# Kernel optimization log

Hardware: AMD Instinct MI355X
Metric: run time of the kernel (lower is better)

Reference implementation:

```python
import jax, jax.numpy as jnp
import numpy as np

B, S, D, H, E, F = 4, 2048, 1024, 16, 8, 4096
CAP_FACTOR = 1.25
DH = D // H


def setup_inputs() -> dict:
    key = jax.random.key(0)
    ks = jax.random.split(key, 8)
    s = 0.02
    return {
        "src": jax.random.normal(ks[0], (B, S, D), jnp.float32),
        "src_pad_mask": jnp.zeros((B, S), jnp.bool_),  # True = padding
        "ln1_g": jnp.ones((D,), jnp.float32),
        "ln1_b": jnp.zeros((D,), jnp.float32),
        "in_proj_w": jax.random.normal(ks[1], (3 * D, D), jnp.float32) * s,
        "in_proj_b": jnp.zeros((3 * D,), jnp.float32),
        "out_proj_w": jax.random.normal(ks[2], (D, D), jnp.float32) * s,
        "out_proj_b": jnp.zeros((D,), jnp.float32),
        "ln2_g": jnp.ones((D,), jnp.float32),
        "ln2_b": jnp.zeros((D,), jnp.float32),
        "router_w": jax.random.normal(ks[3], (D, E), jnp.float32) * s,
        "router_b": jnp.zeros((E,), jnp.float32),
        "w1": jax.random.normal(ks[4], (E, D, F), jnp.float32) * s,
        "b1": jnp.zeros((E, F), jnp.float32),
        "w2": jax.random.normal(ks[5], (E, F, D), jnp.float32) * s,
        "b2": jnp.zeros((E, D), jnp.float32),
    }


def _layernorm(x, g, b, eps=1e-5):
    m = jnp.mean(x, axis=-1, keepdims=True)
    v = jnp.mean(jnp.square(x - m), axis=-1, keepdims=True)
    return (x - m) * jax.lax.rsqrt(v + eps) * g + b


def _mha(x, pad_mask, in_proj_w, in_proj_b, out_proj_w, out_proj_b):
    qkv = x @ in_proj_w.T + in_proj_b                      # [B,S,3D]
    q, k, v = jnp.split(qkv, 3, axis=-1)
    q = q.reshape(B, S, H, DH)
    k = k.reshape(B, S, H, DH)
    v = v.reshape(B, S, H, DH)
    scores = jnp.einsum('bqhd,bkhd->bhqk', q, k) / np.sqrt(DH).astype(np.float32)
    scores = jnp.where(pad_mask[:, None, None, :], jnp.float32(-1e9), scores)
    attn = jax.nn.softmax(scores, axis=-1)
    out = jnp.einsum('bhqk,bkhd->bqhd', attn, v).reshape(B, S, D)
    return out @ out_proj_w.T + out_proj_b


def _switch(x, token_mask, router_w, router_b, w1, b1, w2, b2):
    N = B * S
    cap = int(CAP_FACTOR * N / E)
    tokens = x.reshape(N, D)
    tm = token_mask.reshape(N).astype(jnp.float32)
    logits = tokens @ router_w + router_b                  # [N,E]
    probs = jax.nn.softmax(logits, axis=-1)
    eidx = jnp.argmax(probs, axis=-1)                      # [N] top-1 expert
    gate = jnp.take_along_axis(probs, eidx[:, None], axis=1)[:, 0]
    oh = jax.nn.one_hot(eidx, E, dtype=jnp.float32) * tm[:, None]
    # position of each token within its expert's queue (1-based; 0 if masked)
    pos = jnp.sum(jnp.cumsum(oh, axis=0) * oh, axis=-1)
    keep = (pos > 0) & (pos <= cap)
    slot = eidx * cap + (pos - 1).astype(jnp.int32)        # flat slot in [E*cap)
    slot_scatter = jnp.where(keep, slot, E * cap)          # out-of-range => dropped
    keepf = keep.astype(jnp.float32)
    dispatch = jnp.zeros((E * cap, D), jnp.float32).at[slot_scatter].set(
        tokens * keepf[:, None], mode='drop')
    d = dispatch.reshape(E, cap, D)
    h = jax.nn.relu(jnp.einsum('ecd,edf->ecf', d, w1) + b1[:, None, :])
    o = jnp.einsum('ecf,efd->ecd', h, w2) + b2[:, None, :]
    slot_gather = jnp.where(keep, slot, 0)
    out = o.reshape(E * cap, D)[slot_gather] * (gate * keepf)[:, None]
    # aux losses over valid tokens
    denom = jnp.maximum(jnp.sum(tm), 1.0)
    f = jnp.sum(oh, axis=0) / denom                        # dispatch fraction per expert
    P = jnp.sum(probs * tm[:, None], axis=0) / denom       # mean router prob per expert
    lb_loss = E * jnp.sum(f * P)
    z_loss = jnp.sum(jnp.square(jax.nn.logsumexp(logits, axis=-1)) * tm) / denom
    return out.reshape(B, S, D), lb_loss, z_loss


def reference(src, src_pad_mask, ln1_g, ln1_b, in_proj_w, in_proj_b,
              out_proj_w, out_proj_b, ln2_g, ln2_b, router_w, router_b,
              w1, b1, w2, b2):
    x = _layernorm(src, ln1_g, ln1_b)
    attn = _mha(x, src_pad_mask, in_proj_w, in_proj_b, out_proj_w, out_proj_b)
    src1 = src + attn                                      # dropout=0.0
    token_mask = ~src_pad_mask
    x2 = _layernorm(src1, ln2_g, ln2_b)
    ffn, lb_loss, z_loss = _switch(x2, token_mask, router_w, router_b, w1, b1, w2, b2)
    src2 = src1 + ffn
    return (src2, lb_loss, z_loss)
```

## Files before the change

kernel.cpp:

```cpp
#include <hip/hip_runtime.h>

constexpr int cB = 4, cS = 2048, cD = 1024, cH = 16, cE = 8, cF = 4096;
constexpr int cN = cB * cS;
constexpr int cDH = 64;
constexpr int cCAP = 1280;

typedef __attribute__((ext_vector_type(8))) short bf16x8;
typedef __attribute__((ext_vector_type(4))) float f32x4;
typedef __attribute__((ext_vector_type(4))) unsigned short u16x4;
typedef __attribute__((ext_vector_type(4))) unsigned int u32x4;

__device__ inline unsigned short bf16_rne(float x) {
  unsigned u = __float_as_uint(x);
  u += 0x7FFF + ((u >> 16) & 1);
  return (unsigned short)(u >> 16);
}
__device__ inline float bf16_f(unsigned short h) {
  return __uint_as_float(((unsigned)h) << 16);
}
__device__ inline unsigned cvt_pk_bf16(float a, float b) {
  unsigned r;
  asm("v_cvt_pk_bf16_f32 %0, %1, %2" : "=v"(r) : "v"(a), "v"(b));
  return r;
}

__global__ __launch_bounds__(256) void ln_kernel(const float* __restrict__ x,
                                                 const float* __restrict__ g,
                                                 const float* __restrict__ bb,
                                                 float* __restrict__ y) {
  __shared__ float red[8];
  const int row = blockIdx.x;
  const int t = threadIdx.x;
  const float4 v = ((const float4*)(x + (size_t)row * cD))[t];
  float s = v.x + v.y + v.z + v.w;
#pragma unroll
  for (int m = 32; m >= 1; m >>= 1) s += __shfl_xor(s, m, 64);
  if ((t & 63) == 0) red[t >> 6] = s;
  __syncthreads();
  const float mean = (red[0] + red[1] + red[2] + red[3]) * (1.0f / cD);
  const float dx = v.x - mean, dy = v.y - mean, dz = v.z - mean, dw = v.w - mean;
  float ss = dx * dx + dy * dy + dz * dz + dw * dw;
#pragma unroll
  for (int m = 32; m >= 1; m >>= 1) ss += __shfl_xor(ss, m, 64);
  if ((t & 63) == 0) red[4 + (t >> 6)] = ss;
  __syncthreads();
  const float var = (red[4] + red[5] + red[6] + red[7]) * (1.0f / cD);
  const float inv = rsqrtf(var + 1e-5f);
  const float4 gg = ((const float4*)g)[t];
  const float4 b4 = ((const float4*)bb)[t];
  float4 o;
  o.x = dx * inv * gg.x + b4.x;
  o.y = dy * inv * gg.y + b4.y;
  o.z = dz * inv * gg.z + b4.z;
  o.w = dw * inv * gg.w + b4.w;
  ((float4*)(y + (size_t)row * cD))[t] = o;
}

__global__ __launch_bounds__(256) void ln_split_kernel(
    const float* __restrict__ x, const float* __restrict__ g,
    const float* __restrict__ bb, unsigned short* __restrict__ yh,
    unsigned short* __restrict__ yl) {
  __shared__ float red[8];
  const int row = blockIdx.x;
  const int t = threadIdx.x;
  const float4 v = ((const float4*)(x + (size_t)row * cD))[t];
  float s = v.x + v.y + v.z + v.w;
#pragma unroll
  for (int m = 32; m >= 1; m >>= 1) s += __shfl_xor(s, m, 64);
  if ((t & 63) == 0) red[t >> 6] = s;
  __syncthreads();
  const float mean = (red[0] + red[1] + red[2] + red[3]) * (1.0f / cD);
  const float dx = v.x - mean, dy = v.y - mean, dz = v.z - mean, dw = v.w - mean;
  float ss = dx * dx + dy * dy + dz * dz + dw * dw;
#pragma unroll
  for (int m = 32; m >= 1; m >>= 1) ss += __shfl_xor(ss, m, 64);
  if ((t & 63) == 0) red[4 + (t >> 6)] = ss;
  __syncthreads();
  const float var = (red[4] + red[5] + red[6] + red[7]) * (1.0f / cD);
  const float inv = rsqrtf(var + 1e-5f);
  const float4 gg = ((const float4*)g)[t];
  const float4 b4 = ((const float4*)bb)[t];
  const float oa[4] = {dx * inv * gg.x + b4.x, dy * inv * gg.y + b4.y,
                       dz * inv * gg.z + b4.z, dw * inv * gg.w + b4.w};
  u16x4 hh, ll;
#pragma unroll
  for (int i = 0; i < 4; i++) {
    const unsigned short h16 = bf16_rne(oa[i]);
    hh[i] = h16;
    ll[i] = bf16_rne(oa[i] - bf16_f(h16));
  }
  *(u16x4*)(yh + (size_t)row * cD + t * 4) = hh;
  *(u16x4*)(yl + (size_t)row * cD + t * 4) = ll;
}

__global__ __launch_bounds__(256) void wsplit_kernel(const float* __restrict__ in,
                                                     unsigned short* __restrict__ hi,
                                                     unsigned short* __restrict__ lo,
                                                     int n4) {
  const int i = blockIdx.x * 256 + threadIdx.x;
  if (i >= n4) return;
  const float4 v = ((const float4*)in)[i];
  const float a[4] = {v.x, v.y, v.z, v.w};
  u16x4 hh, ll;
#pragma unroll
  for (int j = 0; j < 4; j++) {
    const unsigned short h16 = bf16_rne(a[j]);
    hh[j] = h16;
    ll[j] = bf16_rne(a[j] - bf16_f(h16));
  }
  *(u16x4*)(hi + (size_t)i * 4) = hh;
  *(u16x4*)(lo + (size_t)i * 4) = ll;
}

__global__ __launch_bounds__(256) void padmask_kernel(
    const unsigned char* __restrict__ pad, float* __restrict__ mkf) {
  const int i = blockIdx.x * 256 + threadIdx.x;
  mkf[i] = pad[i] ? -1e30f : 0.0f;
}

__global__ __launch_bounds__(256) void transpose_bf16_kernel(
    const float* __restrict__ in, unsigned short* __restrict__ outp, int Rr,
    int Cc) {
  __shared__ float T[64][65];
  const int z = blockIdx.z;
  in += (size_t)z * Rr * Cc;
  outp += (size_t)z * Rr * Cc;
  const int c0 = blockIdx.x * 64, r0 = blockIdx.y * 64;
  const int tid = threadIdx.x;
#pragma unroll
  for (int u = 0; u < 4; u++) {
    const int a = tid + u * 256;
    const int r = a >> 4, c4 = (a & 15) << 2;
    const float4 v = *(const float4*)(in + (size_t)(r0 + r) * Cc + c0 + c4);
    T[r][c4 + 0] = v.x;
    T[r][c4 + 1] = v.y;
    T[r][c4 + 2] = v.z;
    T[r][c4 + 3] = v.w;
  }
  __syncthreads();
#pragma unroll
  for (int u = 0; u < 4; u++) {
    const int a = tid + u * 256;
    const int c = a >> 4, r4 = (a & 15) << 2;
    u16x4 o;
#pragma unroll
    for (int i = 0; i < 4; i++) o[i] = bf16_rne(T[r4 + i][c]);
    *(u16x4*)(outp + (size_t)(c0 + c) * Rr + r0 + r4) = o;
  }
}

template <bool SPLIT, bool RELU, bool RESID, int OUT>
__global__ __launch_bounds__(256) void gemm_bf16(
    const unsigned short* __restrict__ Ah, const unsigned short* __restrict__ Al,
    size_t sA,
    const unsigned short* __restrict__ Bh, const unsigned short* __restrict__ Bl,
    size_t sB,
    const float* __restrict__ bias, size_t sBias,
    const float* __restrict__ R,
    void* __restrict__ Cv, size_t sC,
    int K, int lda, int ldb, int ldc,
    unsigned short* __restrict__ Qh, unsigned short* __restrict__ Ql,
    unsigned short* __restrict__ Kh, unsigned short* __restrict__ Kl,
    unsigned short* __restrict__ Vth, unsigned short* __restrict__ Vtl) {
  __shared__ unsigned short AsH[128 * 40];
  __shared__ unsigned short BsH[128 * 40];
  __shared__ unsigned short AsL[SPLIT ? 128 * 40 : 8];
  __shared__ unsigned short BsL[SPLIT ? 128 * 40 : 8];
  const int z = blockIdx.z;
  Ah += (size_t)z * sA;
  Bh += (size_t)z * sB;
  if constexpr (SPLIT) {
    Al += (size_t)z * sA;
    Bl += (size_t)z * sB;
  }
  bias += (size_t)z * sBias;
  const int n0 = blockIdx.x * 128, m0 = blockIdx.y * 128;
  const int tid = threadIdx.x;
  const int wid = tid >> 6, lane = tid & 63;
  const int ln = lane & 15, quad = lane >> 4;
  const int wm = (wid >> 1) * 64, wn = (wid & 1) * 64;

  f32x4 acc[4][4];
#pragma unroll
  for (int i = 0; i < 4; i++)
#pragma unroll
    for (int j = 0; j < 4; j++) acc[i][j] = (f32x4){0.f, 0.f, 0.f, 0.f};

  for (int k0 = 0; k0 < K; k0 += 32) {
    __syncthreads();
#pragma unroll
    for (int u = 0; u < 2; u++) {
      const int c = tid + u * 256;
      const int row = c >> 2, ko = (c & 3) << 3;
      const int ld = row * 40 + ko;
      *(uint4*)&AsH[ld] = *(const uint4*)(Ah + (size_t)(m0 + row) * lda + k0 + ko);
      *(uint4*)&BsH[ld] = *(const uint4*)(Bh + (size_t)(n0 + row) * ldb + k0 + ko);
      if constexpr (SPLIT) {
        *(uint4*)&AsL[ld] = *(const uint4*)(Al + (size_t)(m0 + row) * lda + k0 + ko);
        *(uint4*)&BsL[ld] = *(const uint4*)(Bl + (size_t)(n0 + row) * ldb + k0 + ko);
      }
    }
    __syncthreads();
    bf16x8 bh[4], bl[4];
#pragma unroll
    for (int nt = 0; nt < 4; nt++) {
      bh[nt] = *(const bf16x8*)&BsH[(wn + nt * 16 + ln) * 40 + quad * 8];
      if constexpr (SPLIT)
        bl[nt] = *(const bf16x8*)&BsL[(wn + nt * 16 + ln) * 40 + quad * 8];
    }
#pragma unroll
    for (int mt = 0; mt < 4; mt++) {
      const bf16x8 ah = *(const bf16x8*)&AsH[(wm + mt * 16 + ln) * 40 + quad * 8];
      bf16x8 al;
      if constexpr (SPLIT)
        al = *(const bf16x8*)&AsL[(wm + mt * 16 + ln) * 40 + quad * 8];
#pragma unroll
      for (int nt = 0; nt < 4; nt++) {
        acc[mt][nt] =
            __builtin_amdgcn_mfma_f32_16x16x32_bf16(ah, bh[nt], acc[mt][nt], 0, 0, 0);
        if constexpr (SPLIT) {
          acc[mt][nt] =
              __builtin_amdgcn_mfma_f32_16x16x32_bf16(al, bh[nt], acc[mt][nt], 0, 0, 0);
          acc[mt][nt] =
              __builtin_amdgcn_mfma_f32_16x16x32_bf16(ah, bl[nt], acc[mt][nt], 0, 0, 0);
        }
      }
    }
  }
  if constexpr (OUT == 2) {
#pragma unroll
    for (int mt = 0; mt < 4; mt++) {
      const int row0 = m0 + wm + mt * 16 + quad * 4;
      const int b_ = row0 >> 11, s0_ = row0 & 2047;
      const size_t bbase = (size_t)b_ * cH * cS * cDH;
#pragma unroll
      for (int nt = 0; nt < 4; nt++) {
        const int col = n0 + wn + nt * 16 + ln;
        const float bv = bias[col];
        const int sec = col >> 10;
        const int f = col & 1023;
        const int hh = f >> 6, d = f & 63;
        const size_t bh_off = bbase + (size_t)hh * cS * cDH;
        float vals[4];
#pragma unroll
        for (int r = 0; r < 4; r++) vals[r] = acc[mt][nt][r] + bv;
        if (sec == 2) {
          u16x4 hi4, lo4;
#pragma unroll
          for (int r = 0; r < 4; r++) {
            const unsigned short h16 = bf16_rne(vals[r]);
            hi4[r] = h16;
            lo4[r] = bf16_rne(vals[r] - bf16_f(h16));
          }
          const size_t idx = bh_off + (size_t)d * cS + s0_;
          *(u16x4*)(Vth + idx) = hi4;
          *(u16x4*)(Vtl + idx) = lo4;
        } else {
          unsigned short* dsth = (sec == 0) ? Qh : Kh;
          unsigned short* dstl = (sec == 0) ? Ql : Kl;
#pragma unroll
          for (int r = 0; r < 4; r++) {
            const unsigned short h16 = bf16_rne(vals[r]);
            const size_t idx = bh_off + (size_t)(s0_ + r) * cDH + d;
            dsth[idx] = h16;
            dstl[idx] = bf16_rne(vals[r] - bf16_f(h16));
          }
        }
      }
    }
  } else {
    float* Cf = nullptr;
    unsigned short* Cb = nullptr;
    if constexpr (OUT == 1)
      Cb = (unsigned short*)Cv + (size_t)z * sC;
    else
      Cf = (float*)Cv + (size_t)z * sC;
#pragma unroll
    for (int mt = 0; mt < 4; mt++) {
#pragma unroll
      for (int nt = 0; nt < 4; nt++) {
        const int col = n0 + wn + nt * 16 + ln;
        const float bv = bias[col];
#pragma unroll
        for (int r = 0; r < 4; r++) {
          const int row = m0 + wm + mt * 16 + quad * 4 + r;
          float v = acc[mt][nt][r] + bv;
          if constexpr (RELU) v = fmaxf(v, 0.f);
          if constexpr (RESID) v += R[(size_t)row * ldc + col];
          if constexpr (OUT == 1)
            Cb[(size_t)row * ldc + col] = bf16_rne(v);
          else
            Cf[(size_t)row * ldc + col] = v;
        }
      }
    }
  }
}

__global__ __launch_bounds__(256) void attn_mfma_kernel(
    const unsigned short* __restrict__ Qh, const unsigned short* __restrict__ Ql,
    const unsigned short* __restrict__ Kh, const unsigned short* __restrict__ Kl,
    const unsigned short* __restrict__ Vth, const unsigned short* __restrict__ Vtl,
    const float* __restrict__ mkf, unsigned short* __restrict__ Oh,
    unsigned short* __restrict__ Ol) {
  __shared__ alignas(16) unsigned short KsH[64 * 64];
  __shared__ alignas(16) unsigned short KsL[64 * 64];
  __shared__ alignas(16) unsigned short VsH[64 * 64];
  __shared__ alignas(16) unsigned short VsL[64 * 64];

  const int q0 = blockIdx.x << 6;
  const int h = blockIdx.y, b = blockIdx.z;
  const int tid = threadIdx.x;
  const int wid = tid >> 6, lane = tid & 63;
  const int ln = lane & 15, quad = lane >> 4;
  constexpr float SC2 = 0.125f * 1.4426950408889634f;

  const size_t bh = (size_t)(b * cH + h);
  const unsigned short* gKh = Kh + bh * cS * cDH;
  const unsigned short* gKl = Kl + bh * cS * cDH;
  const unsigned short* gVh = Vth + bh * cDH * cS;
  const unsigned short* gVl = Vtl + bh * cDH * cS;
  const float* gM = mkf + (size_t)b * cS;

  const int t8 = tid & 7;
  const int srow0 = tid >> 3;
  const int srow1 = srow0 + 32;
  const int xw0 = (srow0 & 7) << 4, xw1 = (srow1 & 7) << 4;
  const int wbK0 = srow0 * 128 + ((t8 << 4) ^ xw0);
  const int wbK1 = srow1 * 128 + ((t8 << 4) ^ xw1);
  const int h6 = (t8 >> 2) << 6;
  const int uu = t8 & 3;
  const int pA = h6 + ((((uu & 1) << 2) | (uu >> 1)) << 3);
  const int pB = pA + 16;
  const int wbVA0 = srow0 * 128 + (pA ^ xw0);
  const int wbVB0 = srow0 * 128 + (pB ^ xw0);
  const int wbVA1 = srow1 * 128 + (pA ^ xw1);
  const int wbVB1 = srow1 * 128 + (pB ^ xw1);

  const int xs = (ln & 7) << 4;
  const int fc[2] = {(quad * 16) ^ xs, (quad * 16 + 64) ^ xs};

  const size_t qbase = (bh * cS + q0 + wid * 16 + ln) * cDH;
  bf16x8 qh[2], ql[2];
#pragma unroll
  for (int ks = 0; ks < 2; ks++) {
    qh[ks] = *(const bf16x8*)(Qh + qbase + ks * 32 + quad * 8);
    ql[ks] = *(const bf16x8*)(Ql + qbase + ks * 32 + quad * 8);
  }

  f32x4 Oc[4];
#pragma unroll
  for (int dt = 0; dt < 4; dt++) Oc[dt] = (f32x4){0.f, 0.f, 0.f, 0.f};
  float mprev = -1e30f, lrun = 0.f;

  for (int kt = 0; kt < cS / 64; kt++) {
    const int k0 = kt << 6;
    {
      const size_t kr0 = (size_t)(k0 + srow0) * cDH + (t8 << 3);
      const size_t kr1 = (size_t)(k0 + srow1) * cDH + (t8 << 3);
      *(uint4*)((char*)KsH + wbK0) = *(const uint4*)(gKh + kr0);
      *(uint4*)((char*)KsH + wbK1) = *(const uint4*)(gKh + kr1);
      *(uint4*)((char*)KsL + wbK0) = *(const uint4*)(gKl + kr0);
      *(uint4*)((char*)KsL + wbK1) = *(const uint4*)(gKl + kr1);
      const size_t vr0 = (size_t)srow0 * cS + k0 + (t8 << 3);
      const size_t vr1 = (size_t)srow1 * cS + k0 + (t8 << 3);
      const uint4 a = *(const uint4*)(gVh + vr0);
      const uint4 b2 = *(const uint4*)(gVh + vr1);
      const uint4 c = *(const uint4*)(gVl + vr0);
      const uint4 d = *(const uint4*)(gVl + vr1);
      uint2 t;
      t.x = a.x;  t.y = a.y;  *(uint2*)((char*)VsH + wbVA0) = t;
      t.x = a.z;  t.y = a.w;  *(uint2*)((char*)VsH + wbVB0) = t;
      t.x = b2.x; t.y = b2.y; *(uint2*)((char*)VsH + wbVA1) = t;
      t.x = b2.z; t.y = b2.w; *(uint2*)((char*)VsH + wbVB1) = t;
      t.x = c.x;  t.y = c.y;  *(uint2*)((char*)VsL + wbVA0) = t;
      t.x = c.z;  t.y = c.w;  *(uint2*)((char*)VsL + wbVB0) = t;
      t.x = d.x;  t.y = d.y;  *(uint2*)((char*)VsL + wbVA1) = t;
      t.x = d.z;  t.y = d.w;  *(uint2*)((char*)VsL + wbVB1) = t;
    }
    __syncthreads();

    float sf[4][4];
#pragma unroll
    for (int st = 0; st < 4; st++) {
      f32x4 acc = (f32x4){0.f, 0.f, 0.f, 0.f};
      const char* rH = (const char*)KsH + (st * 16 + ln) * 128;
      const char* rL = (const char*)KsL + (st * 16 + ln) * 128;
#pragma unroll
      for (int ks = 0; ks < 2; ks++) {
        const bf16x8 kh = *(const bf16x8*)(rH + fc[ks]);
        const bf16x8 kl = *(const bf16x8*)(rL + fc[ks]);
        acc = __builtin_amdgcn_mfma_f32_16x16x32_bf16(kh, qh[ks], acc, 0, 0, 0);
        acc = __builtin_amdgcn_mfma_f32_16x16x32_bf16(kl, qh[ks], acc, 0, 0, 0);
        acc = __builtin_amdgcn_mfma_f32_16x16x32_bf16(kh, ql[ks], acc, 0, 0, 0);
      }
      const float4 mkv = *(const float4*)(gM + k0 + st * 16 + quad * 4);
      sf[st][0] = acc[0] * SC2 + mkv.x;
      sf[st][1] = acc[1] * SC2 + mkv.y;
      sf[st][2] = acc[2] * SC2 + mkv.z;
      sf[st][3] = acc[3] * SC2 + mkv.w;
    }
    float vm = sf[0][0];
#pragma unroll
    for (int st = 0; st < 4; st++)
#pragma unroll
      for (int r = 0; r < 4; r++) vm = fmaxf(vm, sf[st][r]);
    if (!__all(vm <= mprev + 8.0f)) {
      float vmr = fmaxf(vm, __shfl_xor(vm, 16, 64));
      vmr = fmaxf(vmr, __shfl_xor(vmr, 32, 64));
      const float mnew = fmaxf(mprev, vmr);
      const float alpha = exp2f(mprev - mnew);
      lrun *= alpha;
#pragma unroll
      for (int dt = 0; dt < 4; dt++) {
        Oc[dt][0] *= alpha;
        Oc[dt][1] *= alpha;
        Oc[dt][2] *= alpha;
        Oc[dt][3] *= alpha;
      }
      mprev = mnew;
    }
    u32x4 ph[2], pl[2];
    float rs = 0.f;
#pragma unroll
    for (int st = 0; st < 4; st++) {
#pragma unroll
      for (int rp = 0; rp < 2; rp++) {
        const float p0 = exp2f(sf[st][2 * rp] - mprev);
        const float p1 = exp2f(sf[st][2 * rp + 1] - mprev);
        rs += p0 + p1;
        const unsigned wh = cvt_pk_bf16(p0, p1);
        const float f0 = __uint_as_float(wh << 16);
        const float f1 = __uint_as_float(wh & 0xFFFF0000u);
        const unsigned wl = cvt_pk_bf16(p0 - f0, p1 - f1);
        ph[st >> 1][(st & 1) * 2 + rp] = wh;
        pl[st >> 1][(st & 1) * 2 + rp] = wl;
      }
    }
    lrun += rs;
    const bf16x8 pbh[2] = {__builtin_bit_cast(bf16x8, ph[0]),
                           __builtin_bit_cast(bf16x8, ph[1])};
    const bf16x8 pbl[2] = {__builtin_bit_cast(bf16x8, pl[0]),
                           __builtin_bit_cast(bf16x8, pl[1])};
#pragma unroll
    for (int dt = 0; dt < 4; dt++) {
      f32x4 acc = Oc[dt];
      const char* vH = (const char*)VsH + (dt * 16 + ln) * 128;
      const char* vL = (const char*)VsL + (dt * 16 + ln) * 128;
#pragma unroll
      for (int ks = 0; ks < 2; ks++) {
        const bf16x8 vh = *(const bf16x8*)(vH + fc[ks]);
        const bf16x8 vl = *(const bf16x8*)(vL + fc[ks]);
        acc = __builtin_amdgcn_mfma_f32_16x16x32_bf16(vh, pbh[ks], acc, 0, 0, 0);
        acc = __builtin_amdgcn_mfma_f32_16x16x32_bf16(vh, pbl[ks], acc, 0, 0, 0);
        acc = __builtin_amdgcn_mfma_f32_16x16x32_bf16(vl, pbh[ks], acc, 0, 0, 0);
      }
      Oc[dt] = acc;
    }
    __syncthreads();
  }
  lrun += __shfl_xor(lrun, 16, 64);
  lrun += __shfl_xor(lrun, 32, 64);
  const float inv = 1.0f / lrun;
  const int tok = b * cS + q0 + wid * 16 + ln;
#pragma unroll
  for (int dt = 0; dt < 4; dt++) {
    u16x4 oh4, ol4;
#pragma unroll
    for (int r = 0; r < 4; r++) {
      const float v = Oc[dt][r] * inv;
      const unsigned short h16 = bf16_rne(v);
      oh4[r] = h16;
      ol4[r] = bf16_rne(v - bf16_f(h16));
    }
    const size_t idx = (size_t)tok * cD + h * cDH + dt * 16 + quad * 4;
    *(u16x4*)(Oh + idx) = oh4;
    *(u16x4*)(Ol + idx) = ol4;
  }
}

__global__ __launch_bounds__(256) void router_kernel(
    const float* __restrict__ x2, const float* __restrict__ rw,
    const float* __restrict__ rb, const unsigned char* __restrict__ pad,
    float* __restrict__ gate, int* __restrict__ eidx, float* __restrict__ Psum,
    float* __restrict__ zsum) {
  __shared__ float Pacc[8];
  __shared__ float Zacc;
  if (threadIdx.x < 8) Pacc[threadIdx.x] = 0.f;
  if (threadIdx.x == 8) Zacc = 0.f;
  __syncthreads();
  const int tid = threadIdx.x, wid = tid >> 6, lane = tid & 63;
  const int e = lane & 7, dbase = lane >> 3;
  for (int tok = blockIdx.x * 4 + wid; tok < cN; tok += gridDim.x * 4) {
    const float* xr = x2 + (size_t)tok * cD;
    float partial = 0.f;
#pragma unroll 8
    for (int i = 0; i < cD / 8; i++) {
      const int d = dbase + i * 8;
      partial += xr[d] * rw[d * 8 + e];
    }
    partial += __shfl_xor(partial, 8, 64);
    partial += __shfl_xor(partial, 16, 64);
    partial += __shfl_xor(partial, 32, 64);
    const float logit = partial + rb[e];
    float mx = logit;
    mx = fmaxf(mx, __shfl_xor(mx, 1, 64));
    mx = fmaxf(mx, __shfl_xor(mx, 2, 64));
    mx = fmaxf(mx, __shfl_xor(mx, 4, 64));
    const float ex = __expf(logit - mx);
    float sm = ex;
    sm += __shfl_xor(sm, 1, 64);
    sm += __shfl_xor(sm, 2, 64);
    sm += __shfl_xor(sm, 4, 64);
    const float prob = ex / sm;
    float bv = logit;
    int bi = e;
#pragma unroll
    for (int m = 1; m < 8; m <<= 1) {
      const float ov = __shfl_xor(bv, m, 64);
      const int oi = __shfl_xor(bi, m, 64);
      if (ov > bv || (ov == bv && oi < bi)) {
        bv = ov;
        bi = oi;
      }
    }
    const float g = __shfl(prob, (lane & 0x38) | bi, 64);
    const bool valid = (pad[tok] == 0);
    if (lane == 0) {
      eidx[tok] = bi;
      gate[tok] = g;
    }
    if (valid) {
      if (lane < 8) atomicAdd(&Pacc[lane], prob);
      if (lane == 0) {
        const float lse = mx + logf(sm);
        atomicAdd(&Zacc, lse * lse);
      }
    }
  }
  __syncthreads();
  if (threadIdx.x < 8) atomicAdd(&Psum[threadIdx.x], Pacc[threadIdx.x]);
  if (threadIdx.x == 8) atomicAdd(zsum, Zacc);
}

__global__ __launch_bounds__(256) void scan_kernel(const int* __restrict__ eidx,
                                                   const unsigned char* __restrict__ pad,
                                                   int* __restrict__ slot,
                                                   int* __restrict__ counts) {
  __shared__ int cnt[256][8];
  const int t = threadIdx.x;
  int lc[8] = {0, 0, 0, 0, 0, 0, 0, 0};
  const int base = t * 32;
  for (int i = 0; i < 32; i++) {
    const int tok = base + i;
    if (!pad[tok]) lc[eidx[tok]]++;
  }
#pragma unroll
  for (int e2 = 0; e2 < 8; e2++) cnt[t][e2] = lc[e2];
  __syncthreads();
  if (t < 8) {
    int run = 0;
    for (int i = 0; i < 256; i++) {
      const int v = cnt[i][t];
      cnt[i][t] = run;
      run += v;
    }
    counts[t] = run;
  }
  __syncthreads();
  int off[8];
#pragma unroll
  for (int e2 = 0; e2 < 8; e2++) off[e2] = cnt[t][e2];
  for (int i = 0; i < 32; i++) {
    const int tok = base + i;
    if (!pad[tok]) {
      const int e2 = eidx[tok];
      const int p = off[e2]++;
      slot[tok] = (p < cCAP) ? (e2 * cCAP + p) : -1;
    } else {
      slot[tok] = -1;
    }
  }
}

__global__ __launch_bounds__(256) void dispatch_bf16_kernel(
    const float* __restrict__ x2, const int* __restrict__ slot,
    unsigned short* __restrict__ disp) {
  const int tok = blockIdx.x;
  const int s = slot[tok];
  if (s < 0) return;
  const float4 v = ((const float4*)(x2 + (size_t)tok * cD))[threadIdx.x];
  u16x4 o;
  o[0] = bf16_rne(v.x);
  o[1] = bf16_rne(v.y);
  o[2] = bf16_rne(v.z);
  o[3] = bf16_rne(v.w);
  *(u16x4*)(disp + (size_t)s * cD + threadIdx.x * 4) = o;
}

__global__ __launch_bounds__(256) void gather_kernel(const float* __restrict__ src1,
                                                     const float* __restrict__ o,
                                                     const int* __restrict__ slot,
                                                     const float* __restrict__ gate,
                                                     float* __restrict__ out) {
  const int tok = blockIdx.x;
  float4 r = ((const float4*)(src1 + (size_t)tok * cD))[threadIdx.x];
  const int s = slot[tok];
  if (s >= 0) {
    const float g = gate[tok];
    const float4 ov = ((const float4*)(o + (size_t)s * cD))[threadIdx.x];
    r.x += g * ov.x;
    r.y += g * ov.y;
    r.z += g * ov.z;
    r.w += g * ov.w;
  }
  ((float4*)(out + (size_t)tok * cD))[threadIdx.x] = r;
}

__global__ void loss_kernel(const int* __restrict__ counts,
                            const float* __restrict__ Psum,
                            const float* __restrict__ zsum,
                            float* __restrict__ out) {
  if (threadIdx.x == 0) {
    int tot = 0;
    for (int e2 = 0; e2 < 8; e2++) tot += counts[e2];
    const float denom = fmaxf((float)tot, 1.0f);
    float lp = 0.f;
    for (int e2 = 0; e2 < 8; e2++)
      lp += ((float)counts[e2] / denom) * (Psum[e2] / denom);
    out[0] = 8.0f * lp;
    out[1] = zsum[0] / denom;
  }
}

constexpr size_t OFF_A = 0;
constexpr size_t OFF_B = 25165824;
constexpr size_t OFF_XHL = 50331648;
constexpr size_t OFF_SRC1 = 58720256;
constexpr size_t OFF_X2O = 67108864;
constexpr size_t OFF_IPW = 77594624;
constexpr size_t OFF_OPW = 80740352;
constexpr size_t OFF_MISC = 81788928;

extern "C" void kernel_launch(void* const* d_in, const int* in_sizes, int n_in,
                              void* d_out, int out_size, void* d_ws, size_t ws_size,
                              hipStream_t stream) {
  (void)in_sizes; (void)n_in; (void)out_size; (void)ws_size;
  const float* src = (const float*)d_in[0];
  const unsigned char* pad = (const unsigned char*)d_in[1];
  const float* ln1_g = (const float*)d_in[2];
  const float* ln1_b = (const float*)d_in[3];
  const float* in_proj_w = (const float*)d_in[4];
  const float* in_proj_b = (const float*)d_in[5];
  const float* out_proj_w = (const float*)d_in[6];
  const float* out_proj_b = (const float*)d_in[7];
  const float* ln2_g = (const float*)d_in[8];
  const float* ln2_b = (const float*)d_in[9];
  const float* router_w = (const float*)d_in[10];
  const float* router_b = (const float*)d_in[11];
  const float* w1 = (const float*)d_in[12];
  const float* b1 = (const float*)d_in[13];
  const float* w2 = (const float*)d_in[14];
  const float* b2 = (const float*)d_in[15];
  float* out = (float*)d_out;
  float* w = (float*)d_ws;

  unsigned short* w1t = (unsigned short*)(w + OFF_A);
  unsigned short* w2t = (unsigned short*)(w + OFF_A);
  unsigned short* usB = (unsigned short*)(w + OFF_B);
  constexpr size_t SPN = (size_t)cN * cD;
  unsigned short* Qh = usB + 0 * SPN;
  unsigned short* Ql = usB + 1 * SPN;
  unsigned short* Kh = usB + 2 * SPN;
  unsigned short* Kl = usB + 3 * SPN;
  unsigned short* Vth = usB + 4 * SPN;
  unsigned short* Vtl = usB + 5 * SPN;
  unsigned short* hbuf16 = usB;
  unsigned short* xh = (unsigned short*)(w + OFF_XHL);
  unsigned short* xl = xh + SPN;
  unsigned short* Oh = xh;
  unsigned short* Ol = xh + SPN;
  unsigned short* disp16 = xh;
  float* src1 = w + OFF_SRC1;
  float* mkf = w + OFF_X2O;
  float* x2 = w + OFF_X2O;
  float* obuf = w + OFF_X2O;
  unsigned short* ipwh = (unsigned short*)(w + OFF_IPW);
  unsigned short* ipwl = ipwh + (size_t)3 * cD * cD;
  unsigned short* opwh = (unsigned short*)(w + OFF_OPW);
  unsigned short* opwl = opwh + (size_t)cD * cD;
  float* gate = w + OFF_MISC;
  int* eidx = (int*)(w + OFF_MISC + 8192);
  int* slot = (int*)(w + OFF_MISC + 16384);
  float* Psum = w + OFF_MISC + 24576;
  float* zsum = Psum + 8;
  int* counts = (int*)(Psum + 16);

  hipMemsetAsync(Psum, 0, 9 * sizeof(float), stream);

  ln_split_kernel<<<cN, 256, 0, stream>>>(src, ln1_g, ln1_b, xh, xl);
  padmask_kernel<<<cN / 256, 256, 0, stream>>>(pad, mkf);
  wsplit_kernel<<<3072, 256, 0, stream>>>(in_proj_w, ipwh, ipwl, 786432);
  wsplit_kernel<<<1024, 256, 0, stream>>>(out_proj_w, opwh, opwl, 262144);
  gemm_bf16<true, false, false, 2><<<dim3(24, 64, 1), 256, 0, stream>>>(
      xh, xl, 0, ipwh, ipwl, 0, in_proj_b, 0, nullptr, nullptr, 0,
      cD, cD, cD, 0, Qh, Ql, Kh, Kl, Vth, Vtl);
  transpose_bf16_kernel<<<dim3(64, 16, 8), 256, 0, stream>>>(w1, w1t, cD, cF);
  attn_mfma_kernel<<<dim3(cS / 64, cH, cB), 256, 0, stream>>>(
      Qh, Ql, Kh, Kl, Vth, Vtl, mkf, Oh, Ol);
  gemm_bf16<true, false, true, 0><<<dim3(8, 64, 1), 256, 0, stream>>>(
      Oh, Ol, 0, opwh, opwl, 0, out_proj_b, 0, src, src1, 0,
      cD, cD, cD, cD, nullptr, nullptr, nullptr, nullptr, nullptr, nullptr);
  ln_kernel<<<cN, 256, 0, stream>>>(src1, ln2_g, ln2_b, x2);
  router_kernel<<<256, 256, 0, stream>>>(x2, router_w, router_b, pad, gate, eidx,
                                         Psum, zsum);
  scan_kernel<<<1, 256, 0, stream>>>(eidx, pad, slot, counts);
  dispatch_bf16_kernel<<<cN, 256, 0, stream>>>(x2, slot, disp16);
  gemm_bf16<false, true, false, 1><<<dim3(32, 10, 8), 256, 0, stream>>>(
      disp16, nullptr, (size_t)cCAP * cD, w1t, nullptr, (size_t)cD * cF,
      b1, cF, nullptr, hbuf16, (size_t)cCAP * cF, cD, cD, cD, cF,
      nullptr, nullptr, nullptr, nullptr, nullptr, nullptr);
  transpose_bf16_kernel<<<dim3(16, 64, 8), 256, 0, stream>>>(w2, w2t, cF, cD);
  gemm_bf16<false, false, false, 0><<<dim3(8, 10, 8), 256, 0, stream>>>(
      hbuf16, nullptr, (size_t)cCAP * cF, w2t, nullptr, (size_t)cF * cD,
      b2, cD, nullptr, obuf, (size_t)cCAP * cD, cF, cF, cF, cD,
      nullptr, nullptr, nullptr, nullptr, nullptr, nullptr);
  gather_kernel<<<cN, 256, 0, stream>>>(src1, obuf, slot, gate, out);
  loss_kernel<<<1, 64, 0, stream>>>(counts, Psum, zsum, out + (size_t)cN * cD);
}
```

Baseline: 1.427 ms.

## Process two 64-row query tiles per attention block to reuse K/V tiles

Result: faster. 1.264 ms (-11.4%).

```diff
diff --git a/kernel.cpp b/kernel.cpp
--- a/kernel.cpp
+++ b/kernel.cpp
@@ -297,6 +297,53 @@
   }
 }
 
+__device__ inline void softmax_pack(const float (&sf)[4][4], float& mprev,
+                                    float& lrun, f32x4 (&Oc)[4],
+                                    bf16x8 (&pbh)[2], bf16x8 (&pbl)[2]) {
+  float vm = sf[0][0];
+#pragma unroll
+  for (int st = 0; st < 4; st++)
+#pragma unroll
+    for (int r = 0; r < 4; r++) vm = fmaxf(vm, sf[st][r]);
+  if (!__all(vm <= mprev + 8.0f)) {
+    float vmr = fmaxf(vm, __shfl_xor(vm, 16, 64));
+    vmr = fmaxf(vmr, __shfl_xor(vmr, 32, 64));
+    const float mnew = fmaxf(mprev, vmr);
+    const float alpha = exp2f(mprev - mnew);
+    lrun *= alpha;
+#pragma unroll
+    for (int dt = 0; dt < 4; dt++) {
+      Oc[dt][0] *= alpha;
+      Oc[dt][1] *= alpha;
+      Oc[dt][2] *= alpha;
+      Oc[dt][3] *= alpha;
+    }
+    mprev = mnew;
+  }
+  u32x4 ph[2], pl[2];
+  float rs = 0.f;
+#pragma unroll
+  for (int st = 0; st < 4; st++) {
+#pragma unroll
+    for (int rp = 0; rp < 2; rp++) {
+      const float p0 = exp2f(sf[st][2 * rp] - mprev);
+      const float p1 = exp2f(sf[st][2 * rp + 1] - mprev);
+      rs += p0 + p1;
+      const unsigned wh = cvt_pk_bf16(p0, p1);
+      const float f0 = __uint_as_float(wh << 16);
+      const float f1 = __uint_as_float(wh & 0xFFFF0000u);
+      const unsigned wl = cvt_pk_bf16(p0 - f0, p1 - f1);
+      ph[st >> 1][(st & 1) * 2 + rp] = wh;
+      pl[st >> 1][(st & 1) * 2 + rp] = wl;
+    }
+  }
+  lrun += rs;
+  pbh[0] = __builtin_bit_cast(bf16x8, ph[0]);
+  pbh[1] = __builtin_bit_cast(bf16x8, ph[1]);
+  pbl[0] = __builtin_bit_cast(bf16x8, pl[0]);
+  pbl[1] = __builtin_bit_cast(bf16x8, pl[1]);
+}
+
 __global__ __launch_bounds__(256) void attn_mfma_kernel(
     const unsigned short* __restrict__ Qh, const unsigned short* __restrict__ Ql,
     const unsigned short* __restrict__ Kh, const unsigned short* __restrict__ Kl,
@@ -308,7 +355,7 @@
   __shared__ alignas(16) unsigned short VsH[64 * 64];
   __shared__ alignas(16) unsigned short VsL[64 * 64];
 
-  const int q0 = blockIdx.x << 6;
+  const int q0 = blockIdx.x << 7;
   const int h = blockIdx.y, b = blockIdx.z;
   const int tid = threadIdx.x;
   const int wid = tid >> 6, lane = tid & 63;
@@ -341,17 +388,23 @@
   const int fc[2] = {(quad * 16) ^ xs, (quad * 16 + 64) ^ xs};
 
   const size_t qbase = (bh * cS + q0 + wid * 16 + ln) * cDH;
-  bf16x8 qh[2], ql[2];
+  bf16x8 qhA[2], qlA[2], qhB[2], qlB[2];
 #pragma unroll
   for (int ks = 0; ks < 2; ks++) {
-    qh[ks] = *(const bf16x8*)(Qh + qbase + ks * 32 + quad * 8);
-    ql[ks] = *(const bf16x8*)(Ql + qbase + ks * 32 + quad * 8);
-  }
-
-  f32x4 Oc[4];
-#pragma unroll
-  for (int dt = 0; dt < 4; dt++) Oc[dt] = (f32x4){0.f, 0.f, 0.f, 0.f};
-  float mprev = -1e30f, lrun = 0.f;
+    qhA[ks] = *(const bf16x8*)(Qh + qbase + ks * 32 + quad * 8);
+    qlA[ks] = *(const bf16x8*)(Ql + qbase + ks * 32 + quad * 8);
+    qhB[ks] = *(const bf16x8*)(Qh + qbase + (size_t)64 * cDH + ks * 32 + quad * 8);
+    qlB[ks] = *(const bf16x8*)(Ql + qbase + (size_t)64 * cDH + ks * 32 + quad * 8);
+  }
+
+  f32x4 OcA[4], OcB[4];
+#pragma unroll
+  for (int dt = 0; dt < 4; dt++) {
+    OcA[dt] = (f32x4){0.f, 0.f, 0.f, 0.f};
+    OcB[dt] = (f32x4){0.f, 0.f, 0.f, 0.f};
+  }
+  float mprevA = -1e30f, lrunA = 0.f;
+  float mprevB = -1e30f, lrunB = 0.f;
 
   for (int kt = 0; kt < cS / 64; kt++) {
     const int k0 = kt << 6;
@@ -380,100 +433,92 @@
     }
     __syncthreads();
 
-    float sf[4][4];
+    float sfA[4][4], sfB[4][4];
 #pragma unroll
     for (int st = 0; st < 4; st++) {
-      f32x4 acc = (f32x4){0.f, 0.f, 0.f, 0.f};
+      f32x4 accA = (f32x4){0.f, 0.f, 0.f, 0.f};
+      f32x4 accB = (f32x4){0.f, 0.f, 0.f, 0.f};
       const char* rH = (const char*)KsH + (st * 16 + ln) * 128;
       const char* rL = (const char*)KsL + (st * 16 + ln) * 128;
 #pragma unroll
       for (int ks = 0; ks < 2; ks++) {
         const bf16x8 kh = *(const bf16x8*)(rH + fc[ks]);
         const bf16x8 kl = *(const bf16x8*)(rL + fc[ks]);
-        acc = __builtin_amdgcn_mfma_f32_16x16x32_bf16(kh, qh[ks], acc, 0, 0, 0);
-        acc = __builtin_amdgcn_mfma_f32_16x16x32_bf16(kl, qh[ks], acc, 0, 0, 0);
-        acc = __builtin_amdgcn_mfma_f32_16x16x32_bf16(kh, ql[ks], acc, 0, 0, 0);
+        accA = __builtin_amdgcn_mfma_f32_16x16x32_bf16(kh, qhA[ks], accA, 0, 0, 0);
+        accB = __builtin_amdgcn_mfma_f32_16x16x32_bf16(kh, qhB[ks], accB, 0, 0, 0);
+        accA = __builtin_amdgcn_mfma_f32_16x16x32_bf16(kl, qhA[ks], accA, 0, 0, 0);
+        accB = __builtin_amdgcn_mfma_f32_16x16x32_bf16(kl, qhB[ks], accB, 0, 0, 0);
+        accA = __builtin_amdgcn_mfma_f32_16x16x32_bf16(kh, qlA[ks], accA, 0, 0, 0);
+        accB = __builtin_amdgcn_mfma_f32_16x16x32_bf16(kh, qlB[ks], accB, 0, 0, 0);
       }
       const float4 mkv = *(const float4*)(gM + k0 + st * 16 + quad * 4);
-      sf[st][0] = acc[0] * SC2 + mkv.x;
-      sf[st][1] = acc[1] * SC2 + mkv.y;
-      sf[st][2] = acc[2] * SC2 + mkv.z;
-      sf[st][3] = acc[3] * SC2 + mkv.w;
-    }
-    float vm = sf[0][0];
-#pragma unroll
-    for (int st = 0; st < 4; st++)
-#pragma unroll
-      for (int r = 0; r < 4; r++) vm = fmaxf(vm, sf[st][r]);
-    if (!__all(vm <= mprev + 8.0f)) {
-      float vmr = fmaxf(vm, __shfl_xor(vm, 16, 64));
-      vmr = fmaxf(vmr, __shfl_xor(vmr, 32, 64));
-      const float mnew = fmaxf(mprev, vmr);
-      const float alpha = exp2f(mprev - mnew);
-      lrun *= alpha;
-#pragma unroll
-      for (int dt = 0; dt < 4; dt++) {
-        Oc[dt][0] *= alpha;
-        Oc[dt][1] *= alpha;
-        Oc[dt][2] *= alpha;
-        Oc[dt][3] *= alpha;
-      }
-      mprev = mnew;
-    }
-    u32x4 ph[2], pl[2];
-    float rs = 0.f;
-#pragma unroll
-    for (int st = 0; st < 4; st++) {
-#pragma unroll
-      for (int rp = 0; rp < 2; rp++) {
-        const float p0 = exp2f(sf[st][2 * rp] - mprev);
-        const float p1 = exp2f(sf[st][2 * rp + 1] - mprev);
-        rs += p0 + p1;
-        const unsigned wh = cvt_pk_bf16(p0, p1);
-        const float f0 = __uint_as_float(wh << 16);
-        const float f1 = __uint_as_float(wh & 0xFFFF0000u);
-        const unsigned wl = cvt_pk_bf16(p0 - f0, p1 - f1);
-        ph[st >> 1][(st & 1) * 2 + rp] = wh;
-        pl[st >> 1][(st & 1) * 2 + rp] = wl;
-      }
-    }
-    lrun += rs;
-    const bf16x8 pbh[2] = {__builtin_bit_cast(bf16x8, ph[0]),
-                           __builtin_bit_cast(bf16x8, ph[1])};
-    const bf16x8 pbl[2] = {__builtin_bit_cast(bf16x8, pl[0]),
-                           __builtin_bit_cast(bf16x8, pl[1])};
+      sfA[st][0] = accA[0] * SC2 + mkv.x;
+      sfA[st][1] = accA[1] * SC2 + mkv.y;
+      sfA[st][2] = accA[2] * SC2 + mkv.z;
+      sfA[st][3] = accA[3] * SC2 + mkv.w;
+      sfB[st][0] = accB[0] * SC2 + mkv.x;
+      sfB[st][1] = accB[1] * SC2 + mkv.y;
+      sfB[st][2] = accB[2] * SC2 + mkv.z;
+      sfB[st][3] = accB[3] * SC2 + mkv.w;
+    }
+    bf16x8 pbhA[2], pblA[2], pbhB[2], pblB[2];
+    softmax_pack(sfA, mprevA, lrunA, OcA, pbhA, pblA);
+    softmax_pack(sfB, mprevB, lrunB, OcB, pbhB, pblB);
 #pragma unroll
     for (int dt = 0; dt < 4; dt++) {
-      f32x4 acc = Oc[dt];
+      f32x4 accA = OcA[dt];
+      f32x4 accB = OcB[dt];
       const char* vH = (const char*)VsH + (dt * 16 + ln) * 128;
       const char* vL = (const char*)VsL + (dt * 16 + ln) * 128;
 #pragma unroll
       for (int ks = 0; ks < 2; ks++) {
         const bf16x8 vh = *(const bf16x8*)(vH + fc[ks]);
         const bf16x8 vl = *(const bf16x8*)(vL + fc[ks]);
-        acc = __builtin_amdgcn_mfma_f32_16x16x32_bf16(vh, pbh[ks], acc, 0, 0, 0);
-        acc = __builtin_amdgcn_mfma_f32_16x16x32_bf16(vh, pbl[ks], acc, 0, 0, 0);
-        acc = __builtin_amdgcn_mfma_f32_16x16x32_bf16(vl, pbh[ks], acc, 0, 0, 0);
+        accA = __builtin_amdgcn_mfma_f32_16x16x32_bf16(vh, pbhA[ks], accA, 0, 0, 0);
+        accB = __builtin_amdgcn_mfma_f32_16x16x32_bf16(vh, pbhB[ks], accB, 0, 0, 0);
+        accA = __builtin_amdgcn_mfma_f32_16x16x32_bf16(vh, pblA[ks], accA, 0, 0, 0);
+        accB = __builtin_amdgcn_mfma_f32_16x16x32_bf16(vh, pblB[ks], accB, 0, 0, 0);
+        accA = __builtin_amdgcn_mfma_f32_16x16x32_bf16(vl, pbhA[ks], accA, 0, 0, 0);
+        accB = __builtin_amdgcn_mfma_f32_16x16x32_bf16(vl, pbhB[ks], accB, 0, 0, 0);
       }
-      Oc[dt] = acc;
+      OcA[dt] = accA;
+      OcB[dt] = accB;
     }
     __syncthreads();
   }
-  lrun += __shfl_xor(lrun, 16, 64);
-  lrun += __shfl_xor(lrun, 32, 64);
-  const float inv = 1.0f / lrun;
-  const int tok = b * cS + q0 + wid * 16 + ln;
+  lrunA += __shfl_xor(lrunA, 16, 64);
+  lrunA += __shfl_xor(lrunA, 32, 64);
+  lrunB += __shfl_xor(lrunB, 16, 64);
+  lrunB += __shfl_xor(lrunB, 32, 64);
+  const float invA = 1.0f / lrunA;
+  const float invB = 1.0f / lrunB;
+  const int tokA = b * cS + q0 + wid * 16 + ln;
+  const int tokB = tokA + 64;
 #pragma unroll
   for (int dt = 0; dt < 4; dt++) {
     u16x4 oh4, ol4;
 #pragma unroll
     for (int r = 0; r < 4; r++) {
-      const float v = Oc[dt][r] * inv;
+      const float v = OcA[dt][r] * invA;
       const unsigned short h16 = bf16_rne(v);
       oh4[r] = h16;
       ol4[r] = bf16_rne(v - bf16_f(h16));
     }
-    const size_t idx = (size_t)tok * cD + h * cDH + dt * 16 + quad * 4;
+    const size_t idx = (size_t)tokA * cD + h * cDH + dt * 16 + quad * 4;
+    *(u16x4*)(Oh + idx) = oh4;
+    *(u16x4*)(Ol + idx) = ol4;
+  }
+#pragma unroll
+  for (int dt = 0; dt < 4; dt++) {
+    u16x4 oh4, ol4;
+#pragma unroll
+    for (int r = 0; r < 4; r++) {
+      const float v = OcB[dt][r] * invB;
+      const unsigned short h16 = bf16_rne(v);
+      oh4[r] = h16;
+      ol4[r] = bf16_rne(v - bf16_f(h16));
+    }
+    const size_t idx = (size_t)tokB * cD + h * cDH + dt * 16 + quad * 4;
     *(u16x4*)(Oh + idx) = oh4;
     *(u16x4*)(Ol + idx) = ol4;
   }
@@ -706,7 +751,7 @@
       xh, xl, 0, ipwh, ipwl, 0, in_proj_b, 0, nullptr, nullptr, 0,
       cD, cD, cD, 0, Qh, Ql, Kh, Kl, Vth, Vtl);
   transpose_bf16_kernel<<<dim3(64, 16, 8), 256, 0, stream>>>(w1, w1t, cD, cF);
-  attn_mfma_kernel<<<dim3(cS / 64, cH, cB), 256, 0, stream>>>(
+  attn_mfma_kernel<<<dim3(cS / 128, cH, cB), 256, 0, stream>>>(
       Qh, Ql, Kh, Kl, Vth, Vtl, mkf, Oh, Ol);
   gemm_bf16<true, false, true, 0><<<dim3(8, 64, 1), 256, 0, stream>>>(
       Oh, Ol, 0, opwh, opwl, 0, out_proj_b, 0, src, src1, 0,
```
